# Performance work log

Measured on AMD Instinct MI355X. Metric: run time of the kernel, lower is better.

Reference implementation:

```python
import jax, jax.numpy as jnp
import numpy as np

B, N, M = 64, 1024, 1024
MAX_ITER = 10      # init default max_iter
EPS = 1e-4         # init default epsilon


def setup_inputs() -> dict:
    key = jax.random.key(0)
    k1, k2, k3 = jax.random.split(key, 3)
    s = jax.random.uniform(k1, (B, N, M), dtype=jnp.float32)
    # ragged valid sizes per batch element, in [N//2, N]
    nrows = jax.random.randint(k2, (B,), N // 2, N + 1, dtype=jnp.int32)
    ncols = jax.random.randint(k3, (B,), M // 2, M + 1, dtype=jnp.int32)
    return {"s": s, "nrows": nrows, "ncols": ncols}


def reference(s, nrows, ncols):
    # Faithful vectorized form of the torch loop:
    #   even iter: sum[b,i,j] = sum_{k<nrows[b]} s[b,k,j]  (masked column sums)
    #   odd  iter: sum[b,i,j] = sum_{k<ncols[b]} s[b,i,k]  (masked row sums)
    #   then s[b,i,j] *= 1/sum inside the [nrows[b], ncols[b]] block, 0 outside.
    Bb, Nn, Mm = s.shape
    row_mask = jnp.arange(Nn)[None, :] < nrows[:, None]          # [B, N]
    col_mask = jnp.arange(Mm)[None, :] < ncols[:, None]          # [B, M]
    block = row_mask[:, :, None] & col_mask[:, None, :]          # [B, N, M]

    s = s + jnp.float32(EPS)
    for i in range(MAX_ITER):
        if i % 2 == 0:
            # column normalization: sum over valid rows
            d = jnp.sum(jnp.where(row_mask[:, :, None], s, 0.0), axis=1, keepdims=True)  # [B,1,M]
            d = jnp.where(col_mask[:, None, :], d, 1.0)  # safe denom outside block
        else:
            # row normalization: sum over valid cols
            d = jnp.sum(jnp.where(col_mask[:, None, :], s, 0.0), axis=2, keepdims=True)  # [B,N,1]
            d = jnp.where(row_mask[:, :, None], d, 1.0)
        s = jnp.where(block, s / d, 0.0)
    return s
```

## Files before the change

### kernel.cpp

```cpp
#include <hip/hip_runtime.h>


#define BB 64
#define NN 1024
#define MM 1024
#define EPS 1e-4f

typedef _Float16 half_t;
typedef __attribute__((ext_vector_type(4))) _Float16 half4_t;
typedef __attribute__((ext_vector_type(8))) _Float16 half8_t;
typedef __attribute__((ext_vector_type(4))) float float4_t;

__global__ __launch_bounds__(256) void prep_kernel(
    const float* __restrict__ s, const int* __restrict__ nrows,
    const int* __restrict__ ncols, half_t* __restrict__ H,
    float* __restrict__ P) {
  int b = blockIdx.z, rc = blockIdx.y, stripe = blockIdx.x;
  int nr = nrows[b], nc = ncols[b];
  float* Pp = P + ((size_t)rc * BB + b) * MM + stripe * 128;
  if (stripe * 128 >= nc) {
    if (threadIdx.x < 128) Pp[threadIdx.x] = 0.f;
    return;
  }
  int tc = threadIdx.x & 31, tr = threadIdx.x >> 5;
  int j0 = stripe * 128 + tc * 4;
  const float* sp = s + (size_t)b * NN * MM + j0;
  half_t* hp = H + (size_t)b * NN * MM + j0;
  float4_t acc = {0.f, 0.f, 0.f, 0.f};
  int base = rc * 128;
#pragma unroll
  for (int it = 0; it < 16; it++) {
    int i = base + it * 8 + tr;
    if (i < nr) {
      float4_t v = *(const float4_t*)(sp + (size_t)i * MM);
      v.x += EPS; v.y += EPS; v.z += EPS; v.w += EPS;
      half4_t h = {(half_t)v.x, (half_t)v.y, (half_t)v.z, (half_t)v.w};
      *(half4_t*)(hp + (size_t)i * MM) = h;
      acc.x += v.x; acc.y += v.y; acc.z += v.z; acc.w += v.w;
    }
  }
  __shared__ float lds[8][128];
  *(float4_t*)&lds[tr][tc * 4] = acc;
  __syncthreads();
  if (threadIdx.x < 128) {
    float s0 = 0.f;
#pragma unroll
    for (int k = 0; k < 8; k++) s0 += lds[k][threadIdx.x];
    Pp[threadIdx.x] = s0;
  }
}

__global__ __launch_bounds__(256) void creduce_kernel(
    const float* __restrict__ P, const int* __restrict__ ncols,
    float* __restrict__ C) {
  int b = blockIdx.y;
  int j = blockIdx.x * 256 + threadIdx.x;
  int nc = ncols[b];
  float s0 = 0.f;
#pragma unroll
  for (int k = 0; k < 8; k++) s0 += P[((size_t)k * BB + b) * MM + j];
  C[b * MM + j] = (j < nc) ? 1.f / s0 : 0.f;
}

__global__ __launch_bounds__(256) void row_kernel(
    const half_t* __restrict__ H, const int* __restrict__ nrows,
    const int* __restrict__ ncols, const float* __restrict__ C,
    float* __restrict__ R) {
  int b = blockIdx.y;
  int nr = nrows[b], nc = ncols[b];
  int l = threadIdx.x & 63;
  int rg = blockIdx.x * 4 + (threadIdx.x >> 6);
  const float* Cp = C + b * MM;
  float4_t c00 = *(const float4_t*)(Cp + l * 8);
  float4_t c01 = *(const float4_t*)(Cp + l * 8 + 4);
  float4_t c10 = *(const float4_t*)(Cp + 512 + l * 8);
  float4_t c11 = *(const float4_t*)(Cp + 512 + l * 8 + 4);
  bool hi = (512 + l * 8) < nc;
  const half_t* hp = H + (size_t)b * NN * MM + l * 8;
#pragma unroll
  for (int r = 0; r < 8; r++) {
    int i = rg + (r << 7);
    if (i < nr) {
      const half_t* hr = hp + (size_t)i * MM;
      half8_t h0 = *(const half8_t*)hr;
      float acc = (float)h0[0] * c00.x + (float)h0[1] * c00.y +
                  (float)h0[2] * c00.z + (float)h0[3] * c00.w +
                  (float)h0[4] * c01.x + (float)h0[5] * c01.y +
                  (float)h0[6] * c01.z + (float)h0[7] * c01.w;
      if (hi) {
        half8_t h1 = *(const half8_t*)(hr + 512);
        acc += (float)h1[0] * c10.x + (float)h1[1] * c10.y +
               (float)h1[2] * c10.z + (float)h1[3] * c10.w +
               (float)h1[4] * c11.x + (float)h1[5] * c11.y +
               (float)h1[6] * c11.z + (float)h1[7] * c11.w;
      }
#pragma unroll
      for (int off = 32; off > 0; off >>= 1) acc += __shfl_xor(acc, off, 64);
      if (l == 0) R[b * NN + i] = 1.f / acc;
    }
  }
}

__global__ __launch_bounds__(256) void col_kernel(
    const half_t* __restrict__ H, const int* __restrict__ nrows,
    const int* __restrict__ ncols, const float* __restrict__ R,
    float* __restrict__ C) {
  int b = blockIdx.y;
  int j0 = blockIdx.x * 64;
  int nr = nrows[b], nc = ncols[b];
  if (j0 >= nc) {
    if (threadIdx.x < 64) C[b * MM + j0 + threadIdx.x] = 0.f;
    return;
  }
  int tc = threadIdx.x & 7, tr = threadIdx.x >> 3;
  const half_t* hp = H + (size_t)b * NN * MM + j0 + tc * 8;
  const float* Rp = R + b * NN;
  float acc[8] = {0.f, 0.f, 0.f, 0.f, 0.f, 0.f, 0.f, 0.f};
#pragma unroll 4
  for (int it = 0; it < 32; it++) {
    int i = (it << 5) + tr;
    if (i < nr) {
      half8_t h = *(const half8_t*)(hp + (size_t)i * MM);
      float r = Rp[i];
#pragma unroll
      for (int k = 0; k < 8; k++) acc[k] += (float)h[k] * r;
    }
  }
  __shared__ float lds[32][64];
#pragma unroll
  for (int k = 0; k < 8; k++) lds[tr][tc * 8 + k] = acc[k];
  __syncthreads();
  if (threadIdx.x < 64) {
    float s0 = 0.f;
#pragma unroll
    for (int k = 0; k < 32; k++) s0 += lds[k][threadIdx.x];
    int j = j0 + threadIdx.x;
    C[b * MM + j] = (j < nc) ? 1.f / s0 : 0.f;
  }
}

__global__ __launch_bounds__(256) void final_kernel(
    const float* __restrict__ s, const int* __restrict__ nrows,
    const int* __restrict__ ncols, const float* __restrict__ C,
    float* __restrict__ out) {
  int b = blockIdx.y;
  int nr = nrows[b], nc = ncols[b];
  int w = threadIdx.x >> 6, l = threadIdx.x & 63;
  int i = blockIdx.x * 4 + w;
  float* op = out + ((size_t)b * NN + i) * MM;
  float4_t z = {0.f, 0.f, 0.f, 0.f};
  if (i >= nr) {
#pragma unroll
    for (int ch = 0; ch < 4; ch++) *(float4_t*)(op + ch * 256 + l * 4) = z;
    return;
  }
  const float* sp = s + ((size_t)b * NN + i) * MM;
  const float* Cp = C + b * MM;
  float4_t sv[4], cv[4];
  float acc = 0.f;
  int nch = (nc + 255) >> 8;
#pragma unroll
  for (int ch = 0; ch < 4; ch++) {
    if (ch < nch) {
      float4_t v = *(const float4_t*)(sp + ch * 256 + l * 4);
      v.x += EPS; v.y += EPS; v.z += EPS; v.w += EPS;
      sv[ch] = v;
      float4_t c = *(const float4_t*)(Cp + ch * 256 + l * 4);
      cv[ch] = c;
      acc += v.x * c.x + v.y * c.y + v.z * c.z + v.w * c.w;
    }
  }
#pragma unroll
  for (int off = 32; off > 0; off >>= 1) acc += __shfl_xor(acc, off, 64);
  float r = 1.f / acc;
#pragma unroll
  for (int ch = 0; ch < 4; ch++) {
    if (ch < nch) {
      float4_t o;
      o.x = sv[ch].x * cv[ch].x * r;
      o.y = sv[ch].y * cv[ch].y * r;
      o.z = sv[ch].z * cv[ch].z * r;
      o.w = sv[ch].w * cv[ch].w * r;
      *(float4_t*)(op + ch * 256 + l * 4) = o;
    } else {
      *(float4_t*)(op + ch * 256 + l * 4) = z;
    }
  }
}

extern "C" void kernel_launch(void* const* d_in, const int* in_sizes, int n_in,
                              void* d_out, int out_size, void* d_ws,
                              size_t ws_size, hipStream_t stream) {
  const float* s = (const float*)d_in[0];
  const int* nrows = (const int*)d_in[1];
  const int* ncols = (const int*)d_in[2];
  float* out = (float*)d_out;
  half_t* H = (half_t*)d_out;
  float* R = (float*)d_ws;
  float* C = R + BB * NN;
  float* P = C + BB * MM;

  dim3 pgrid(8, 8, BB);
  dim3 dgrid(4, BB);
  dim3 rgrid(32, BB);
  dim3 cgrid(16, BB);
  dim3 fgrid(NN / 4, BB);

  prep_kernel<<<pgrid, 256, 0, stream>>>(s, nrows, ncols, H, P);
  creduce_kernel<<<dgrid, 256, 0, stream>>>(P, ncols, C);
  for (int t = 0; t < 4; t++) {
    row_kernel<<<rgrid, 256, 0, stream>>>(H, nrows, ncols, C, R);
    col_kernel<<<cgrid, 256, 0, stream>>>(H, nrows, ncols, R, C);
  }
  final_kernel<<<fgrid, 256, 0, stream>>>(s, nrows, ncols, C, out);
}
```

Measured before the change: 593.6 us.

## Fuse row and column normalization passes into a single read of the fp16 matrix

Each alternating pair of row and column reductions now runs in one kernel. It computes each row's reciprocal sum and accumulates the row-scaled values into per-chunk column partials, which a small reduce kernel then combines. This halves the passes over the fp16 copy of the matrix per iteration pair. The cost is a coarser grid (8 chunks per batch with 512 threads), which may lower occupancy and parallelism, plus an extra partial-sum buffer and reduce launch.

```diff
diff --git a/kernel.cpp b/kernel.cpp
--- a/kernel.cpp
+++ b/kernel.cpp
@@ -10,6 +10,7 @@
 typedef __attribute__((ext_vector_type(4))) _Float16 half4_t;
 typedef __attribute__((ext_vector_type(8))) _Float16 half8_t;
 typedef __attribute__((ext_vector_type(4))) float float4_t;
+typedef __attribute__((ext_vector_type(2))) float float2_t;
 
 __global__ __launch_bounds__(256) void prep_kernel(
     const float* __restrict__ s, const int* __restrict__ nrows,
@@ -62,81 +63,71 @@
   C[b * MM + j] = (j < nc) ? 1.f / s0 : 0.f;
 }
 
-__global__ __launch_bounds__(256) void row_kernel(
+__global__ __launch_bounds__(512) void fused_kernel(
     const half_t* __restrict__ H, const int* __restrict__ nrows,
     const int* __restrict__ ncols, const float* __restrict__ C,
-    float* __restrict__ R) {
-  int b = blockIdx.y;
+    float* __restrict__ P) {
+  int b = blockIdx.y, ch = blockIdx.x;
   int nr = nrows[b], nc = ncols[b];
-  int l = threadIdx.x & 63;
-  int rg = blockIdx.x * 4 + (threadIdx.x >> 6);
+  int l = threadIdx.x & 63, w = threadIdx.x >> 6;
   const float* Cp = C + b * MM;
-  float4_t c00 = *(const float4_t*)(Cp + l * 8);
-  float4_t c01 = *(const float4_t*)(Cp + l * 8 + 4);
-  float4_t c10 = *(const float4_t*)(Cp + 512 + l * 8);
-  float4_t c11 = *(const float4_t*)(Cp + 512 + l * 8 + 4);
+  float c0[8], c1[8];
+  *(float4_t*)&c0[0] = *(const float4_t*)(Cp + l * 8);
+  *(float4_t*)&c0[4] = *(const float4_t*)(Cp + l * 8 + 4);
+  *(float4_t*)&c1[0] = *(const float4_t*)(Cp + 512 + l * 8);
+  *(float4_t*)&c1[4] = *(const float4_t*)(Cp + 512 + l * 8 + 4);
   bool hi = (512 + l * 8) < nc;
   const half_t* hp = H + (size_t)b * NN * MM + l * 8;
-#pragma unroll
-  for (int r = 0; r < 8; r++) {
-    int i = rg + (r << 7);
+  float a0[8] = {0.f, 0.f, 0.f, 0.f, 0.f, 0.f, 0.f, 0.f};
+  float a1[8] = {0.f, 0.f, 0.f, 0.f, 0.f, 0.f, 0.f, 0.f};
+  int rbase = ch * 128 + w;
+#pragma unroll 4
+  for (int r = 0; r < 16; r++) {
+    int i = rbase + (r << 3);
     if (i < nr) {
       const half_t* hr = hp + (size_t)i * MM;
       half8_t h0 = *(const half8_t*)hr;
-      float acc = (float)h0[0] * c00.x + (float)h0[1] * c00.y +
-                  (float)h0[2] * c00.z + (float)h0[3] * c00.w +
-                  (float)h0[4] * c01.x + (float)h0[5] * c01.y +
-                  (float)h0[6] * c01.z + (float)h0[7] * c01.w;
+      float f0[8];
+#pragma unroll
+      for (int k = 0; k < 8; k++) f0[k] = (float)h0[k];
+      float acc = f0[0] * c0[0] + f0[1] * c0[1] + f0[2] * c0[2] +
+                  f0[3] * c0[3] + f0[4] * c0[4] + f0[5] * c0[5] +
+                  f0[6] * c0[6] + f0[7] * c0[7];
+      float f1[8];
       if (hi) {
         half8_t h1 = *(const half8_t*)(hr + 512);
-        acc += (float)h1[0] * c10.x + (float)h1[1] * c10.y +
-               (float)h1[2] * c10.z + (float)h1[3] * c10.w +
-               (float)h1[4] * c11.x + (float)h1[5] * c11.y +
-               (float)h1[6] * c11.z + (float)h1[7] * c11.w;
+#pragma unroll
+        for (int k = 0; k < 8; k++) f1[k] = (float)h1[k];
+        acc += f1[0] * c1[0] + f1[1] * c1[1] + f1[2] * c1[2] +
+               f1[3] * c1[3] + f1[4] * c1[4] + f1[5] * c1[5] +
+               f1[6] * c1[6] + f1[7] * c1[7];
       }
 #pragma unroll
       for (int off = 32; off > 0; off >>= 1) acc += __shfl_xor(acc, off, 64);
-      if (l == 0) R[b * NN + i] = 1.f / acc;
-    }
-  }
-}
-
-__global__ __launch_bounds__(256) void col_kernel(
-    const half_t* __restrict__ H, const int* __restrict__ nrows,
-    const int* __restrict__ ncols, const float* __restrict__ R,
-    float* __restrict__ C) {
-  int b = blockIdx.y;
-  int j0 = blockIdx.x * 64;
-  int nr = nrows[b], nc = ncols[b];
-  if (j0 >= nc) {
-    if (threadIdx.x < 64) C[b * MM + j0 + threadIdx.x] = 0.f;
-    return;
-  }
-  int tc = threadIdx.x & 7, tr = threadIdx.x >> 3;
-  const half_t* hp = H + (size_t)b * NN * MM + j0 + tc * 8;
-  const float* Rp = R + b * NN;
-  float acc[8] = {0.f, 0.f, 0.f, 0.f, 0.f, 0.f, 0.f, 0.f};
-#pragma unroll 4
-  for (int it = 0; it < 32; it++) {
-    int i = (it << 5) + tr;
-    if (i < nr) {
-      half8_t h = *(const half8_t*)(hp + (size_t)i * MM);
-      float r = Rp[i];
-#pragma unroll
-      for (int k = 0; k < 8; k++) acc[k] += (float)h[k] * r;
-    }
-  }
-  __shared__ float lds[32][64];
-#pragma unroll
-  for (int k = 0; k < 8; k++) lds[tr][tc * 8 + k] = acc[k];
+      float rv = 1.f / acc;
+#pragma unroll
+      for (int k = 0; k < 8; k++) a0[k] += f0[k] * rv;
+      if (hi) {
+#pragma unroll
+        for (int k = 0; k < 8; k++) a1[k] += f1[k] * rv;
+      }
+    }
+  }
+  __shared__ float lds[8][MM];
+#pragma unroll
+  for (int k = 0; k < 8; k++) lds[w][l * 8 + k] = a0[k];
+#pragma unroll
+  for (int k = 0; k < 8; k++) lds[w][512 + l * 8 + k] = a1[k];
   __syncthreads();
-  if (threadIdx.x < 64) {
-    float s0 = 0.f;
-#pragma unroll
-    for (int k = 0; k < 32; k++) s0 += lds[k][threadIdx.x];
-    int j = j0 + threadIdx.x;
-    C[b * MM + j] = (j < nc) ? 1.f / s0 : 0.f;
-  }
+  int t = threadIdx.x;
+  float s0 = 0.f, s1 = 0.f;
+#pragma unroll
+  for (int k = 0; k < 8; k++) {
+    s0 += lds[k][t * 2];
+    s1 += lds[k][t * 2 + 1];
+  }
+  float2_t o = {s0, s1};
+  *(float2_t*)(P + ((size_t)ch * BB + b) * MM + t * 2) = o;
 }
 
 __global__ __launch_bounds__(256) void final_kernel(
@@ -196,21 +187,19 @@
   const int* ncols = (const int*)d_in[2];
   float* out = (float*)d_out;
   half_t* H = (half_t*)d_out;
-  float* R = (float*)d_ws;
-  float* C = R + BB * NN;
+  float* C = (float*)d_ws;
   float* P = C + BB * MM;
 
   dim3 pgrid(8, 8, BB);
   dim3 dgrid(4, BB);
-  dim3 rgrid(32, BB);
-  dim3 cgrid(16, BB);
+  dim3 ugrid(8, BB);
   dim3 fgrid(NN / 4, BB);
 
   prep_kernel<<<pgrid, 256, 0, stream>>>(s, nrows, ncols, H, P);
   creduce_kernel<<<dgrid, 256, 0, stream>>>(P, ncols, C);
   for (int t = 0; t < 4; t++) {
-    row_kernel<<<rgrid, 256, 0, stream>>>(H, nrows, ncols, C, R);
-    col_kernel<<<cgrid, 256, 0, stream>>>(H, nrows, ncols, R, C);
+    fused_kernel<<<ugrid, 512, 0, stream>>>(H, nrows, ncols, C, P);
+    creduce_kernel<<<dgrid, 256, 0, stream>>>(P, ncols, C);
   }
   final_kernel<<<fgrid, 256, 0, stream>>>(s, nrows, ncols, C, out);
 }
```

Result: faster. 566.4 us (-4.6%).
